# Kernel optimization log

Hardware: AMD Instinct MI355X
Metric: run time of the kernel (lower is better)

Reference implementation:

```python
import jax, jax.numpy as jnp
import numpy as np

B, L, K, H, D = 2, 512, 128, 32, 1024
NUM_EDGES = 2048
SQRT_2PI = 2.5066282746310002
MIN_F32 = float(np.finfo(np.float32).min)
SCALING = K ** -0.5


def setup_inputs() -> dict:
    key = jax.random.key(0)
    ks = jax.random.split(key, 18)
    pos = jax.random.normal(ks[0], (B, L, 3), jnp.float32) * 10.0
    node_type_edge = jax.random.randint(ks[1], (B, L, L, 2), 0, NUM_EDGES)
    adj = jax.random.randint(ks[2], (B, L, L), 0, 2).astype(bool)
    # last 64 tokens of second sample are padding
    padding_mask = jnp.arange(L)[None, :] >= jnp.array([L, L - 64])[:, None]
    molecule_mask = jax.random.randint(ks[3], (B, L), 0, 2).astype(bool)
    clean_mask = jax.random.randint(ks[4], (B, L), 0, 2).astype(bool)
    # parameters
    pos_emb_w = jax.random.normal(ks[5], (K, 3), jnp.float32) * 0.1            # nn.Linear(3, K, bias=False)
    pos_feature_emb_w = jax.random.normal(ks[6], (D, K), jnp.float32) * (K ** -0.5)  # nn.Linear(K, D, bias=False)
    gbf_means = jax.random.uniform(ks[7], (K,), jnp.float32, minval=0.0, maxval=3.0)
    gbf_stds = jax.random.uniform(ks[8], (K,), jnp.float32, minval=0.1, maxval=3.0)
    gbf_mul = jax.random.normal(ks[9], (NUM_EDGES, 1), jnp.float32) * 0.1 + 1.0
    gbf_bias = jax.random.normal(ks[10], (NUM_EDGES, 1), jnp.float32) * 0.1
    proj_w1 = jax.random.normal(ks[11], (K, K), jnp.float32) * (K ** -0.5)     # NonLinear layer1
    proj_b1 = jnp.zeros((K,), jnp.float32)
    proj_w2 = jax.random.normal(ks[12], (H, K), jnp.float32) * (K ** -0.5)     # NonLinear layer2
    proj_b2 = jnp.zeros((H,), jnp.float32)
    pos_proj_w = jax.random.normal(ks[13], (D, K), jnp.float32) * (K ** -0.5)  # pos_embedding_proj
    pos_proj_b = jnp.zeros((D,), jnp.float32)
    return dict(pos=pos, node_type_edge=node_type_edge, adj=adj, padding_mask=padding_mask,
                molecule_mask=molecule_mask, clean_mask=clean_mask,
                pos_emb_w=pos_emb_w, pos_feature_emb_w=pos_feature_emb_w,
                gbf_means=gbf_means, gbf_stds=gbf_stds, gbf_mul=gbf_mul, gbf_bias=gbf_bias,
                proj_w1=proj_w1, proj_b1=proj_b1, proj_w2=proj_w2, proj_b2=proj_b2,
                pos_proj_w=pos_proj_w, pos_proj_b=pos_proj_b)


def reference(pos, node_type_edge, adj, padding_mask, molecule_mask, clean_mask,
              pos_emb_w, pos_feature_emb_w, gbf_means, gbf_stds, gbf_mul, gbf_bias,
              proj_w1, proj_b1, proj_w2, proj_b2, pos_proj_w, pos_proj_b):
    # pairwise distances [B,L,L] (eps-safe sqrt; grad at diagonal is 0)
    delta = pos[:, :, None, :] - pos[:, None, :, :]
    dist0 = jnp.sqrt(jnp.sum(delta * delta, axis=-1) + 1e-12)

    # adj forced True on non-molecule / clean rows
    adj = jnp.where(~molecule_mask[:, :, None], True, adj)
    adj = jnp.where(clean_mask[:, :, None], True, adj)

    # GaussianLayer: per-edge-type affine on dist, then K gaussian kernels -> [B,L,L,K]
    mul = gbf_mul[node_type_edge].sum(axis=-2)    # [B,L,L,1]
    bia = gbf_bias[node_type_edge].sum(axis=-2)   # [B,L,L,1]
    x = mul * dist0[..., None] + bia              # [B,L,L,1]
    std = jnp.abs(gbf_stds) + 1e-5                # [K]
    edge_feature = jnp.exp(-0.5 * jnp.square((x - gbf_means) / std)) / (SQRT_2PI * std)  # [B,L,L,K]

    # NonLinear projection to heads
    h = jax.nn.gelu(jnp.einsum('blmk,jk->blmj', edge_feature, proj_w1) + proj_b1, approximate=False)
    gab = jnp.einsum('blmj,nj->blmn', h, proj_w2) + proj_b2   # [B,L,L,H]

    expand_mask = padding_mask
    gab = jnp.where(expand_mask[:, None, :, None], -jnp.inf, gab)
    gab = jnp.where(~adj[..., None], -jnp.inf, gab)
    gab = jnp.where(padding_mask[:, :, None, None], 0.0, gab)
    graph_attn_bias = jnp.transpose(gab, (0, 3, 1, 2))        # [B,H,L,L]

    dist = graph_attn_bias.sum(axis=1)                        # [B,L,L]
    dist = jnp.where(expand_mask[:, None, :], MIN_F32, dist)
    dist = jnp.where(padding_mask[:, :, None], MIN_F32, dist)

    pos_emb = jnp.einsum('blc,kc->blk', pos, pos_emb_w)       # [B,L,K]
    pos_emb = jnp.where(expand_mask[..., None], 0.0, pos_emb)

    dist = jnp.where(~adj, MIN_F32, dist)
    dist = jax.nn.softmax(dist.astype(jnp.float32) * SCALING, axis=-1)

    pfe = jnp.einsum('blm,bmk->blk', dist, pos_emb)           # weighted aggregation
    pfe = jnp.einsum('blk,dk->bld', pfe, pos_feature_emb_w)   # Linear(K, D, bias=False)

    ef = jnp.where(expand_mask[:, None, :, None], 0.0, edge_feature).sum(axis=-2)  # [B,L,K]
    pfe = pfe + jnp.einsum('blk,dk->bld', ef, pos_proj_w) + pos_proj_b
    pfe = jnp.where(padding_mask[..., None], 0.0, pfe)
    return pfe, graph_attn_bias
```

## Files before the change

kernel.cpp:

```cpp
#include <hip/hip_runtime.h>
#include <hip/hip_bf16.h>

typedef __attribute__((ext_vector_type(8))) short short8;
typedef __attribute__((ext_vector_type(4))) float f32x4;

static const int BB = 2;
static const int LL = 512;
#define MIN_F32 (-3.4028234663852886e+38f)
#define NEG_BIG (-1.0e38f)
#define SCALING_F 0.08838834764831845f
#define SQ2PI 2.5066282746310002f

__device__ __forceinline__ float exp2_hw(float x) {
    float r; asm("v_exp_f32 %0, %1" : "=v"(r) : "v"(x)); return r;
}
__device__ __forceinline__ float gelu_fast(float x) {
    float s  = x * 0.70710678118654752440f;
    float za = fabsf(s);
    float t  = __builtin_amdgcn_rcpf(fmaf(za, 0.3275911f, 1.0f));
    float p  = t * fmaf(t, fmaf(t, fmaf(t, fmaf(t, 1.061405429f, -1.453152027f),
                                        1.421413741f), -0.284496736f), 0.254829592f);
    float e  = __expf(-za * za);
    float q  = fmaf(-p, e, 1.0f);
    union { float f; unsigned u; } uq, us;
    uq.f = q; us.f = s;
    uq.u = (uq.u & 0x7FFFFFFFu) | (us.u & 0x80000000u);
    float hx = 0.5f * x;
    return fmaf(hx, uq.f, hx);
}
__device__ __forceinline__ unsigned pack_bf16x2(float lo, float hi) {
    __hip_bfloat162 h2 = __float22bfloat162_rn(float2{lo, hi});
    union { __hip_bfloat162 h; unsigned u; } v; v.h = h2;
    return v.u;
}
__device__ __forceinline__ unsigned short f2bf(float f) {
    union { float f; unsigned int u; } v; v.f = f;
    unsigned int u = v.u;
    return (unsigned short)((u + 0x7FFFu + ((u >> 16) & 1u)) >> 16);
}
__device__ __forceinline__ int swz(int row, int bytecol) {
    return row * 256 + (bytecol ^ ((row & 7) << 4));
}

__global__ __launch_bounds__(512, 4) void row_kernel(
    const float* __restrict__ pos,
    const int*   __restrict__ nte,
    const unsigned char* __restrict__ adj,
    const unsigned char* __restrict__ padm,
    const unsigned char* __restrict__ molm,
    const unsigned char* __restrict__ clnm,
    const float* __restrict__ gmean,
    const float* __restrict__ gstd,
    const float* __restrict__ gmul,
    const float* __restrict__ gbias,
    const float* __restrict__ w1,
    const float* __restrict__ b1,
    const float* __restrict__ w2,
    const float* __restrict__ b2,
    const float* __restrict__ pw,
    const float* __restrict__ wfe,
    const float* __restrict__ wp,
    float* __restrict__ out_gab,
    float* __restrict__ pfe1,
    float* __restrict__ efsum,
    float* __restrict__ wfet,
    float* __restrict__ wpt)
{
    const int t = threadIdx.x;

    if (blockIdx.x >= 1024) {
        int bid = blockIdx.x - 1024;
        #pragma unroll
        for (int q = 0; q < 4; ++q) {
            int idx = bid * 2048 + q * 512 + t;
            int which = idx >> 17;
            int r = idx & 131071;
            int k = r >> 10;
            int d = r & 1023;
            if (which == 0) wfet[r] = wfe[d * 128 + k];
            else            wpt[r]  = wp[d * 128 + k];
        }
        return;
    }

    __shared__ __align__(16) char W1s[128 * 256];
    __shared__ __align__(16) char W2s[32 * 256];
    __shared__ __align__(16) char efs[64 * 256];
    __shared__ __align__(16) char hs [64 * 256];
    __shared__ float dist_row[512];
    __shared__ float xval[512];
    __shared__ unsigned char flgall[512];
    __shared__ float b1s[128];
    __shared__ float b2s[32];
    __shared__ float sred[16];
    __shared__ float dsump[128];
    __shared__ float gelu_tab[384];

    const int row = blockIdx.x;
    const int b = row >> 9;
    const int i = row & 511;

    const int w  = t >> 6;
    const int l  = t & 63;
    const int lr = l & 15;
    const int lq = l >> 4;

    for (int idx = t; idx < 2048 + 512; idx += 512) {
        const float* src; char* dst; int r16, c16;
        if (idx < 2048) { r16 = idx >> 4;          c16 = idx & 15; src = w1 + r16 * 128 + c16 * 8; dst = W1s; }
        else            { r16 = (idx - 2048) >> 4; c16 = (idx - 2048) & 15; src = w2 + r16 * 128 + c16 * 8; dst = W2s; }
        float4 f0 = *(const float4*)(src);
        float4 f1 = *(const float4*)(src + 4);
        uint4 pk;
        pk.x = (unsigned)f2bf(f0.x) | ((unsigned)f2bf(f0.y) << 16);
        pk.y = (unsigned)f2bf(f0.z) | ((unsigned)f2bf(f0.w) << 16);
        pk.z = (unsigned)f2bf(f1.x) | ((unsigned)f2bf(f1.y) << 16);
        pk.w = (unsigned)f2bf(f1.z) | ((unsigned)f2bf(f1.w) << 16);
        *(uint4*)(dst + swz(r16, c16 * 16)) = pk;
    }
    if (t < 128) b1s[t] = b1[t];
    if (t < 32)  b2s[t] = b2[t];
    if (t < 384) gelu_tab[t] = gelu_fast((t - 192) * 0.03125f);

    const bool pad_i = padm[row] != 0;
    const bool force_adj = (clnm[row] != 0) || (molm[row] == 0);
    const float pix = pos[row * 3 + 0], piy = pos[row * 3 + 1], piz = pos[row * 3 + 2];

    {
        int2 e2 = ((const int2*)nte)[row * 512 + t];
        float mul = gmul[e2.x] + gmul[e2.y];
        float bia = gbias[e2.x] + gbias[e2.y];
        float dx = pix - pos[(b * 512 + t) * 3 + 0];
        float dy = piy - pos[(b * 512 + t) * 3 + 1];
        float dz = piz - pos[(b * 512 + t) * 3 + 2];
        float dist = sqrtf(dx * dx + dy * dy + dz * dz + 1e-12f);
        xval[t] = mul * dist + bia;
        int padj = padm[b * 512 + t] ? 1 : 0;
        int adje = (force_adj || adj[row * 512 + t]) ? 2 : 0;
        flgall[t] = (unsigned char)(padj | adje);
    }

    const int k0 = (t & 15) * 8;
    const int js = t >> 4;
    float mean_q[8], istd_q[8], lnc_q[8], efacc[8];
    #pragma unroll
    for (int q = 0; q < 8; ++q) {
        float gsv = fabsf(gstd[k0 + q]) + 1e-5f;
        mean_q[q] = gmean[k0 + q];
        istd_q[q] = 0.84932180f / gsv;
        lnc_q[q]  = -log2f(SQ2PI * gsv);
        efacc[q]  = 0.f;
    }

    auto gelu_lut = [&](float x) -> float {
        float xc = fminf(fmaxf(x, -6.0f), 6.0f);
        float f  = fminf(fmaf(xc, 32.0f, 192.0f), 382.99f);
        float ff = floorf(f);
        float fr = f - ff;
        int idx = (int)ff;
        float v0 = gelu_tab[idx];
        float v1 = gelu_tab[idx + 1];
        float r = fmaf(fr, v1 - v0, v0);
        return x > 5.9f ? x : r;
    };

    __syncthreads();

    for (int tile = 0; tile < 8; ++tile) {
        const int j0 = tile * 64;
        if (tile > 0 && t < 64) {
            int fl = flgall[j0 - 64 + t];
            bool masked = pad_i || (fl & 1) || !(fl & 2);
            dist_row[j0 - 64 + t] = masked ? MIN_F32 : (dsump[t] + dsump[64 + t]);
        }
        #pragma unroll
        for (int jj = 0; jj < 2; ++jj) {
            int j = js + jj * 32;
            float x  = xval[j0 + j];
            float mk = (flgall[j0 + j] & 1) ? 0.0f : 1.0f;
            unsigned pk[4];
            #pragma unroll
            for (int q = 0; q < 4; ++q) {
                float a0 = (x - mean_q[2*q+0]) * istd_q[2*q+0];
                float a1 = (x - mean_q[2*q+1]) * istd_q[2*q+1];
                float e0 = exp2_hw(fmaf(a0, -a0, lnc_q[2*q+0]));
                float e1 = exp2_hw(fmaf(a1, -a1, lnc_q[2*q+1]));
                efacc[2*q+0] = fmaf(e0, mk, efacc[2*q+0]);
                efacc[2*q+1] = fmaf(e1, mk, efacc[2*q+1]);
                pk[q] = pack_bf16x2(e0, e1);
            }
            *(uint4*)(efs + swz(j, 2 * k0)) = make_uint4(pk[0], pk[1], pk[2], pk[3]);
        }
        __syncthreads();
        {
            const int jobase = (w & 3) * 32;
            const int jbase  = (w >> 2) * 32;
            f32x4 a00 = {0.f,0.f,0.f,0.f}, a01 = a00, a10 = a00, a11 = a00;
            #pragma unroll
            for (int ks = 0; ks < 4; ++ks) {
                int bcol = ks * 64 + lq * 16;
                short8 av0 = *(const short8*)(W1s + swz(jobase + lr, bcol));
                short8 av1 = *(const short8*)(W1s + swz(jobase + 16 + lr, bcol));
                short8 bv0 = *(const short8*)(efs + swz(jbase + lr, bcol));
                short8 bv1 = *(const short8*)(efs + swz(jbase + 16 + lr, bcol));
                a00 = __builtin_amdgcn_mfma_f32_16x16x32_bf16(av0, bv0, a00, 0, 0, 0);
                a01 = __builtin_amdgcn_mfma_f32_16x16x32_bf16(av0, bv1, a01, 0, 0, 0);
                a10 = __builtin_amdgcn_mfma_f32_16x16x32_bf16(av1, bv0, a10, 0, 0, 0);
                a11 = __builtin_amdgcn_mfma_f32_16x16x32_bf16(av1, bv1, a11, 0, 0, 0);
            }
            #pragma unroll
            for (int mi = 0; mi < 2; ++mi) {
                int jo0 = jobase + mi * 16 + lq * 4;
                float4 bb = *(const float4*)&b1s[jo0];
                #pragma unroll
                for (int ci = 0; ci < 2; ++ci) {
                    f32x4 acc = (mi == 0) ? (ci == 0 ? a00 : a01) : (ci == 0 ? a10 : a11);
                    int j = jbase + ci * 16 + lr;
                    float g0 = gelu_lut(acc[0] + bb.x);
                    float g1 = gelu_lut(acc[1] + bb.y);
                    float g2 = gelu_lut(acc[2] + bb.z);
                    float g3 = gelu_lut(acc[3] + bb.w);
                    uint2 pv = make_uint2(pack_bf16x2(g0, g1), pack_bf16x2(g2, g3));
                    *(uint2*)(hs + swz(j, 2 * jo0)) = pv;
                }
            }
        }
        __syncthreads();
        {
            const int mt = w >> 2;
            const int jt2 = w & 3;
            f32x4 acc = (f32x4){0.f, 0.f, 0.f, 0.f};
            #pragma unroll
            for (int ks = 0; ks < 4; ++ks) {
                int bcol = ks * 64 + lq * 16;
                short8 av = *(const short8*)(W2s + swz(mt * 16 + lr, bcol));
                short8 bv = *(const short8*)(hs + swz(jt2 * 16 + lr, bcol));
                acc = __builtin_amdgcn_mfma_f32_16x16x32_bf16(av, bv, acc, 0, 0, 0);
            }
            int jl = jt2 * 16 + lr;
            int jg = j0 + jl;
            int fl = flgall[jg];
            bool kill = (fl & 1) || !(fl & 2);
            float dpart = 0.f;
            size_t base = ((size_t)(b * 32 + mt * 16 + lq * 4) * 512 + i) * 512 + jg;
            #pragma unroll
            for (int r = 0; r < 4; ++r) {
                float raw = acc[r] + b2s[mt * 16 + lq * 4 + r];
                dpart += raw;
                float outv = pad_i ? 0.0f : (kill ? NEG_BIG : raw);
                out_gab[base + (size_t)r * 262144] = outv;
            }
            dpart += __shfl_xor(dpart, 16);
            dpart += __shfl_xor(dpart, 32);
            if (l < 16) dsump[mt * 64 + jl] = dpart;
        }
        __syncthreads();
    }

    float* rb = (float*)efs;
    if (t < 64) {
        int fl = flgall[448 + t];
        bool masked = pad_i || (fl & 1) || !(fl & 2);
        dist_row[448 + t] = masked ? MIN_F32 : (dsump[t] + dsump[64 + t]);
    }
    *(float4*)&rb[t * 8 + 0] = make_float4(efacc[0], efacc[1], efacc[2], efacc[3]);
    *(float4*)&rb[t * 8 + 4] = make_float4(efacc[4], efacc[5], efacc[6], efacc[7]);
    __syncthreads();
    if (t < 128) {
        float s = 0.f;
        #pragma unroll
        for (int sidx = 0; sidx < 32; ++sidx) s += rb[sidx * 128 + t];
        efsum[(size_t)row * 128 + t] = s;
    }

    float sv = dist_row[t] * SCALING_F;
    float v = sv;
    #pragma unroll
    for (int m = 32; m > 0; m >>= 1) v = fmaxf(v, __shfl_xor(v, m));
    if ((t & 63) == 0) sred[t >> 6] = v;
    __syncthreads();
    float mx = sred[0];
    #pragma unroll
    for (int w8 = 1; w8 < 8; ++w8) mx = fmaxf(mx, sred[w8]);
    float e = expf(sv - mx);
    v = e;
    #pragma unroll
    for (int m = 32; m > 0; m >>= 1) v += __shfl_xor(v, m);
    if ((t & 63) == 0) sred[8 + (t >> 6)] = v;
    __syncthreads();
    float sm = 0.f;
    #pragma unroll
    for (int w8 = 0; w8 < 8; ++w8) sm += sred[8 + w8];
    float p = e / sm;

    float px = pos[(b * 512 + t) * 3 + 0];
    float py = pos[(b * 512 + t) * 3 + 1];
    float pz = pos[(b * 512 + t) * 3 + 2];
    float vx = p * px, vy = p * py, vz = p * pz;
    #pragma unroll
    for (int m = 32; m > 0; m >>= 1) {
        vx += __shfl_xor(vx, m); vy += __shfl_xor(vy, m); vz += __shfl_xor(vz, m);
    }
    __syncthreads();
    if ((t & 63) == 0) {
        int w8 = t >> 6;
        rb[w8] = vx; rb[8 + w8] = vy; rb[16 + w8] = vz;
    }
    __syncthreads();
    if (t < 128) {
        float w0 = 0.f, w1v = 0.f, w2v = 0.f;
        #pragma unroll
        for (int w8 = 0; w8 < 8; ++w8) {
            w0 += rb[w8]; w1v += rb[8 + w8]; w2v += rb[16 + w8];
        }
        pfe1[(size_t)row * 128 + t] = pw[t * 3 + 0] * w0 + pw[t * 3 + 1] * w1v + pw[t * 3 + 2] * w2v;
    }
}

__global__ __launch_bounds__(256) void pfe_kernel(
    const float* __restrict__ pfe1,
    const float* __restrict__ efsum,
    const float* __restrict__ wfet,
    const float* __restrict__ wpt,
    const float* __restrict__ pb,
    const unsigned char* __restrict__ padm,
    float* __restrict__ out)
{
    __shared__ __align__(16) float As[2 * 32 * 132];
    __shared__ __align__(16) float Bs[2 * 16 * 128];
    const int t  = threadIdx.x;
    const int tx = t & 31;
    const int ty = t >> 5;
    const int r0 = (blockIdx.x >> 3) * 32;
    const int d0 = (blockIdx.x & 7) * 128;

    #pragma unroll
    for (int q = 0; q < 16; ++q) {
        int ii = t + q * 256;
        int r = ii >> 7, k = ii & 127;
        As[(0 * 32 + r) * 132 + k] = pfe1 [(size_t)(r0 + r) * 128 + k];
        As[(1 * 32 + r) * 132 + k] = efsum[(size_t)(r0 + r) * 128 + k];
    }

    f32x4 acc[4];
    #pragma unroll
    for (int rr = 0; rr < 4; ++rr) acc[rr] = (f32x4){0.f, 0.f, 0.f, 0.f};

    for (int kc = 0; kc < 8; ++kc) {
        __syncthreads();
        #pragma unroll
        for (int q = 0; q < 2; ++q) {
            int ii = t + q * 256;
            int kr = ii >> 5, dq = ii & 31;
            f32x4 v0 = ((const f32x4*)(wfet + (size_t)(kc * 16 + kr) * 1024 + d0))[dq];
            f32x4 v1 = ((const f32x4*)(wpt  + (size_t)(kc * 16 + kr) * 1024 + d0))[dq];
            *(f32x4*)&Bs[(0 * 16 + kr) * 128 + dq * 4] = v0;
            *(f32x4*)&Bs[(1 * 16 + kr) * 128 + dq * 4] = v1;
        }
        __syncthreads();
        #pragma unroll
        for (int k4 = 0; k4 < 4; ++k4) {
            int kb = kc * 16 + k4 * 4;
            f32x4 a0[4], a1[4];
            #pragma unroll
            for (int rr = 0; rr < 4; ++rr) {
                int r = ty * 4 + rr;
                a0[rr] = *(const f32x4*)&As[(0 * 32 + r) * 132 + kb];
                a1[rr] = *(const f32x4*)&As[(1 * 32 + r) * 132 + kb];
            }
            #pragma unroll
            for (int kq = 0; kq < 4; ++kq) {
                f32x4 b0 = *(const f32x4*)&Bs[(0 * 16 + k4 * 4 + kq) * 128 + tx * 4];
                f32x4 b1 = *(const f32x4*)&Bs[(1 * 16 + k4 * 4 + kq) * 128 + tx * 4];
                #pragma unroll
                for (int rr = 0; rr < 4; ++rr) {
                    acc[rr] += a0[rr][kq] * b0 + a1[rr][kq] * b1;
                }
            }
        }
    }

    f32x4 bv = *(const f32x4*)&pb[d0 + tx * 4];
    #pragma unroll
    for (int rr = 0; rr < 4; ++rr) {
        int row = r0 + ty * 4 + rr;
        f32x4 o = acc[rr] + bv;
        if (padm[row]) o = (f32x4){0.f, 0.f, 0.f, 0.f};
        *(f32x4*)&out[(size_t)row * 1024 + d0 + tx * 4] = o;
    }
}

extern "C" void kernel_launch(void* const* d_in, const int* in_sizes, int n_in,
                              void* d_out, int out_size, void* d_ws, size_t ws_size,
                              hipStream_t stream) {
    const float* pos  = (const float*)d_in[0];
    const int*   nte  = (const int*)d_in[1];
    const unsigned char* adj  = (const unsigned char*)d_in[2];
    const unsigned char* padm = (const unsigned char*)d_in[3];
    const unsigned char* molm = (const unsigned char*)d_in[4];
    const unsigned char* clnm = (const unsigned char*)d_in[5];
    const float* pw    = (const float*)d_in[6];
    const float* wfe   = (const float*)d_in[7];
    const float* gmean = (const float*)d_in[8];
    const float* gstd  = (const float*)d_in[9];
    const float* gmul  = (const float*)d_in[10];
    const float* gbias = (const float*)d_in[11];
    const float* w1    = (const float*)d_in[12];
    const float* b1    = (const float*)d_in[13];
    const float* w2    = (const float*)d_in[14];
    const float* b2    = (const float*)d_in[15];
    const float* wp    = (const float*)d_in[16];
    const float* pb    = (const float*)d_in[17];

    float* out      = (float*)d_out;
    float* out_pfe  = out;
    float* out_gab  = out + (size_t)BB * LL * 1024;

    float* ws    = (float*)d_ws;
    float* pfe1  = ws;
    float* efsum = ws + 131072;
    float* wfet  = ws + 262144;
    float* wpt   = ws + 393216;

    row_kernel<<<BB * LL + 128, 512, 0, stream>>>(pos, nte, adj, padm, molm, clnm,
                                                  gmean, gstd, gmul, gbias,
                                                  w1, b1, w2, b2, pw, wfe, wp,
                                                  out_gab, pfe1, efsum, wfet, wpt);
    pfe_kernel<<<256, 256, 0, stream>>>(pfe1, efsum, wfet, wpt, pb, padm, out_pfe);
}
```

Measured before the change: 103.5 us.

## Keep MLP weight fragments in registers and vectorize graph bias stores

W1 and W2 are now loaded straight from global memory into per-wave bf16 MFMA fragments held in registers, instead of being staged through 40KB of swizzled shared memory. This cuts LDS footprint and per-tile LDS reads, which may allow more blocks per CU. The second GEMM swaps its operands so each lane holds four consecutive j values, so the [B,H,L,L] bias writes become float4 stores; the head-sum reduction changes to 16-lane shuffles to match. The Gaussian exponent is also rewritten as a quadratic polynomial in x with precomputed coefficients. The costs are higher register pressure under launch_bounds(512,4), and the expanded quadratic may lose some floating-point accuracy.

```diff
diff --git a/kernel.cpp b/kernel.cpp
--- a/kernel.cpp
+++ b/kernel.cpp
@@ -32,11 +32,6 @@
     __hip_bfloat162 h2 = __float22bfloat162_rn(float2{lo, hi});
     union { __hip_bfloat162 h; unsigned u; } v; v.h = h2;
     return v.u;
-}
-__device__ __forceinline__ unsigned short f2bf(float f) {
-    union { float f; unsigned int u; } v; v.f = f;
-    unsigned int u = v.u;
-    return (unsigned short)((u + 0x7FFFu + ((u >> 16) & 1u)) >> 16);
 }
 __device__ __forceinline__ int swz(int row, int bytecol) {
     return row * 256 + (bytecol ^ ((row & 7) << 4));
@@ -83,13 +78,11 @@
         return;
     }
 
-    __shared__ __align__(16) char W1s[128 * 256];
-    __shared__ __align__(16) char W2s[32 * 256];
     __shared__ __align__(16) char efs[64 * 256];
     __shared__ __align__(16) char hs [64 * 256];
     __shared__ float dist_row[512];
     __shared__ float xval[512];
-    __shared__ unsigned char flgall[512];
+    __shared__ __align__(4) unsigned char flgall[512];
     __shared__ float b1s[128];
     __shared__ float b2s[32];
     __shared__ float sred[16];
@@ -105,22 +98,38 @@
     const int lr = l & 15;
     const int lq = l >> 4;
 
-    for (int idx = t; idx < 2048 + 512; idx += 512) {
-        const float* src; char* dst; int r16, c16;
-        if (idx < 2048) { r16 = idx >> 4;          c16 = idx & 15; src = w1 + r16 * 128 + c16 * 8; dst = W1s; }
-        else            { r16 = (idx - 2048) >> 4; c16 = (idx - 2048) & 15; src = w2 + r16 * 128 + c16 * 8; dst = W2s; }
-        float4 f0 = *(const float4*)(src);
-        float4 f1 = *(const float4*)(src + 4);
-        uint4 pk;
-        pk.x = (unsigned)f2bf(f0.x) | ((unsigned)f2bf(f0.y) << 16);
-        pk.y = (unsigned)f2bf(f0.z) | ((unsigned)f2bf(f0.w) << 16);
-        pk.z = (unsigned)f2bf(f1.x) | ((unsigned)f2bf(f1.y) << 16);
-        pk.w = (unsigned)f2bf(f1.z) | ((unsigned)f2bf(f1.w) << 16);
-        *(uint4*)(dst + swz(r16, c16 * 16)) = pk;
-    }
+    const int jobase = (w & 3) * 32;
+    const int jbase  = (w >> 2) * 32;
+    const int mt  = w >> 2;
+    const int jt2 = w & 3;
+
     if (t < 128) b1s[t] = b1[t];
     if (t < 32)  b2s[t] = b2[t];
     if (t < 384) gelu_tab[t] = gelu_fast((t - 192) * 0.03125f);
+
+    short8 w1f0[4], w1f1[4], w2f[4];
+    {
+        const float* r0p = w1 + (jobase + lr) * 128;
+        const float* r1p = w1 + (jobase + 16 + lr) * 128;
+        const float* r2p = w2 + (mt * 16 + lr) * 128;
+        #pragma unroll
+        for (int ks = 0; ks < 4; ++ks) {
+            int off = ks * 32 + lq * 8;
+            union { uint4 u; short8 s; } cv;
+            float4 x0 = *(const float4*)(r0p + off), x1 = *(const float4*)(r0p + off + 4);
+            cv.u = make_uint4(pack_bf16x2(x0.x, x0.y), pack_bf16x2(x0.z, x0.w),
+                              pack_bf16x2(x1.x, x1.y), pack_bf16x2(x1.z, x1.w));
+            w1f0[ks] = cv.s;
+            float4 y0 = *(const float4*)(r1p + off), y1 = *(const float4*)(r1p + off + 4);
+            cv.u = make_uint4(pack_bf16x2(y0.x, y0.y), pack_bf16x2(y0.z, y0.w),
+                              pack_bf16x2(y1.x, y1.y), pack_bf16x2(y1.z, y1.w));
+            w1f1[ks] = cv.s;
+            float4 z0 = *(const float4*)(r2p + off), z1 = *(const float4*)(r2p + off + 4);
+            cv.u = make_uint4(pack_bf16x2(z0.x, z0.y), pack_bf16x2(z0.z, z0.w),
+                              pack_bf16x2(z1.x, z1.y), pack_bf16x2(z1.z, z1.w));
+            w2f[ks] = cv.s;
+        }
+    }
 
     const bool pad_i = padm[row] != 0;
     const bool force_adj = (clnm[row] != 0) || (molm[row] == 0);
@@ -142,14 +151,17 @@
 
     const int k0 = (t & 15) * 8;
     const int js = t >> 4;
-    float mean_q[8], istd_q[8], lnc_q[8], efacc[8];
+    float Aq[8], Bq[8], Cq[8], efacc[8];
     #pragma unroll
     for (int q = 0; q < 8; ++q) {
         float gsv = fabsf(gstd[k0 + q]) + 1e-5f;
-        mean_q[q] = gmean[k0 + q];
-        istd_q[q] = 0.84932180f / gsv;
-        lnc_q[q]  = -log2f(SQ2PI * gsv);
-        efacc[q]  = 0.f;
+        float mn  = gmean[k0 + q];
+        float is  = 0.84932180f / gsv;
+        float s   = is * is;
+        Aq[q] = -s;
+        Bq[q] = 2.0f * mn * s;
+        Cq[q] = -log2f(SQ2PI * gsv) - mn * mn * s;
+        efacc[q] = 0.f;
     }
 
     auto gelu_lut = [&](float x) -> float {
@@ -181,10 +193,8 @@
             unsigned pk[4];
             #pragma unroll
             for (int q = 0; q < 4; ++q) {
-                float a0 = (x - mean_q[2*q+0]) * istd_q[2*q+0];
-                float a1 = (x - mean_q[2*q+1]) * istd_q[2*q+1];
-                float e0 = exp2_hw(fmaf(a0, -a0, lnc_q[2*q+0]));
-                float e1 = exp2_hw(fmaf(a1, -a1, lnc_q[2*q+1]));
+                float e0 = exp2_hw(fmaf(x, fmaf(x, Aq[2*q+0], Bq[2*q+0]), Cq[2*q+0]));
+                float e1 = exp2_hw(fmaf(x, fmaf(x, Aq[2*q+1], Bq[2*q+1]), Cq[2*q+1]));
                 efacc[2*q+0] = fmaf(e0, mk, efacc[2*q+0]);
                 efacc[2*q+1] = fmaf(e1, mk, efacc[2*q+1]);
                 pk[q] = pack_bf16x2(e0, e1);
@@ -193,20 +203,16 @@
         }
         __syncthreads();
         {
-            const int jobase = (w & 3) * 32;
-            const int jbase  = (w >> 2) * 32;
             f32x4 a00 = {0.f,0.f,0.f,0.f}, a01 = a00, a10 = a00, a11 = a00;
             #pragma unroll
             for (int ks = 0; ks < 4; ++ks) {
                 int bcol = ks * 64 + lq * 16;
-                short8 av0 = *(const short8*)(W1s + swz(jobase + lr, bcol));
-                short8 av1 = *(const short8*)(W1s + swz(jobase + 16 + lr, bcol));
                 short8 bv0 = *(const short8*)(efs + swz(jbase + lr, bcol));
                 short8 bv1 = *(const short8*)(efs + swz(jbase + 16 + lr, bcol));
-                a00 = __builtin_amdgcn_mfma_f32_16x16x32_bf16(av0, bv0, a00, 0, 0, 0);
-                a01 = __builtin_amdgcn_mfma_f32_16x16x32_bf16(av0, bv1, a01, 0, 0, 0);
-                a10 = __builtin_amdgcn_mfma_f32_16x16x32_bf16(av1, bv0, a10, 0, 0, 0);
-                a11 = __builtin_amdgcn_mfma_f32_16x16x32_bf16(av1, bv1, a11, 0, 0, 0);
+                a00 = __builtin_amdgcn_mfma_f32_16x16x32_bf16(w1f0[ks], bv0, a00, 0, 0, 0);
+                a01 = __builtin_amdgcn_mfma_f32_16x16x32_bf16(w1f0[ks], bv1, a01, 0, 0, 0);
+                a10 = __builtin_amdgcn_mfma_f32_16x16x32_bf16(w1f1[ks], bv0, a10, 0, 0, 0);
+                a11 = __builtin_amdgcn_mfma_f32_16x16x32_bf16(w1f1[ks], bv1, a11, 0, 0, 0);
             }
             #pragma unroll
             for (int mi = 0; mi < 2; ++mi) {
@@ -227,32 +233,36 @@
         }
         __syncthreads();
         {
-            const int mt = w >> 2;
-            const int jt2 = w & 3;
             f32x4 acc = (f32x4){0.f, 0.f, 0.f, 0.f};
             #pragma unroll
             for (int ks = 0; ks < 4; ++ks) {
-                int bcol = ks * 64 + lq * 16;
-                short8 av = *(const short8*)(W2s + swz(mt * 16 + lr, bcol));
-                short8 bv = *(const short8*)(hs + swz(jt2 * 16 + lr, bcol));
-                acc = __builtin_amdgcn_mfma_f32_16x16x32_bf16(av, bv, acc, 0, 0, 0);
-            }
-            int jl = jt2 * 16 + lr;
-            int jg = j0 + jl;
-            int fl = flgall[jg];
-            bool kill = (fl & 1) || !(fl & 2);
-            float dpart = 0.f;
-            size_t base = ((size_t)(b * 32 + mt * 16 + lq * 4) * 512 + i) * 512 + jg;
+                short8 af = *(const short8*)(hs + swz(jt2 * 16 + lr, ks * 64 + lq * 16));
+                acc = __builtin_amdgcn_mfma_f32_16x16x32_bf16(af, w2f[ks], acc, 0, 0, 0);
+            }
+            int n  = mt * 16 + lr;
+            int jl = jt2 * 16 + lq * 4;
+            int jq = j0 + jl;
+            float bb = b2s[n];
+            f32x4 raw;
+            #pragma unroll
+            for (int r = 0; r < 4; ++r) raw[r] = acc[r] + bb;
+            f32x4 red = raw;
+            #pragma unroll
+            for (int m = 1; m <= 8; m <<= 1) {
+                #pragma unroll
+                for (int r = 0; r < 4; ++r) red[r] += __shfl_xor(red[r], m);
+            }
+            if (lr == 0)
+                *(float4*)&dsump[mt * 64 + jl] = make_float4(red[0], red[1], red[2], red[3]);
+            unsigned fl4 = *(const unsigned*)&flgall[jq];
+            f32x4 ov;
             #pragma unroll
             for (int r = 0; r < 4; ++r) {
-                float raw = acc[r] + b2s[mt * 16 + lq * 4 + r];
-                dpart += raw;
-                float outv = pad_i ? 0.0f : (kill ? NEG_BIG : raw);
-                out_gab[base + (size_t)r * 262144] = outv;
-            }
-            dpart += __shfl_xor(dpart, 16);
-            dpart += __shfl_xor(dpart, 32);
-            if (l < 16) dsump[mt * 64 + jl] = dpart;
+                int fl = (fl4 >> (8 * r)) & 255;
+                bool kill = (fl & 1) || !(fl & 2);
+                ov[r] = pad_i ? 0.0f : (kill ? NEG_BIG : raw[r]);
+            }
+            *(f32x4*)&out_gab[((size_t)(b * 32 + n) * 512 + i) * 512 + jq] = ov;
         }
         __syncthreads();
     }
```

Result: slower. 177.7 us (+71.6%).
